# Kernel tuning notes

Measured on AMD Instinct MI355X. Metric: run time of the kernel, lower is better.

## Reference

```python
import jax, jax.numpy as jnp
import numpy as np

N_NODES = 50000
IN_C, HID_C, OUT_C = 128, 128, 64
N_EDGES = 800000


def setup_inputs() -> dict:
    key = jax.random.key(0)
    k1, k2, k3, k4, k5, k6 = jax.random.split(key, 6)
    x = jax.random.normal(k1, (N_NODES, IN_C), dtype=jnp.float32)
    edge_index = jax.random.randint(k2, (2, N_EDGES), 0, N_NODES, dtype=jnp.int64)
    # Glorot-ish init for the two GCN layer weights + biases
    W1 = jax.random.normal(k3, (IN_C, HID_C), dtype=jnp.float32) / np.sqrt(IN_C)
    b1 = jnp.zeros((HID_C,), dtype=jnp.float32)
    W2 = jax.random.normal(k4, (HID_C, OUT_C), dtype=jnp.float32) / np.sqrt(HID_C)
    b2 = jnp.zeros((OUT_C,), dtype=jnp.float32)
    return {"x": x, "edge_index": edge_index, "W1": W1, "b1": b1, "W2": W2, "b2": b2}


def _gcn_norm(edge_index, num_nodes):
    # Add self-loops, then symmetric normalization: deg^-1/2[row] * deg^-1/2[col]
    loops = jnp.arange(num_nodes, dtype=edge_index.dtype)
    row = jnp.concatenate([edge_index[0], loops])  # target nodes
    col = jnp.concatenate([edge_index[1], loops])  # source nodes
    ones = jnp.ones(row.shape[0], dtype=jnp.float32)
    deg = jax.ops.segment_sum(ones, row, num_segments=num_nodes)
    dinv = jnp.where(deg > 0, jax.lax.rsqrt(jnp.maximum(deg, 1.0)), 0.0)
    norm = dinv[row] * dinv[col]  # [E + N]
    return row, col, norm


def _gcn_conv(x, row, col, norm, W, b, num_nodes):
    h = x @ W                              # [N, C_out] — transform first (fewer FLOPs)
    msg = h[col] * norm[:, None]           # gather + scale  [E+N, C_out]
    out = jax.ops.segment_sum(msg, row, num_segments=num_nodes)  # scatter-add
    return out + b


def reference(x, edge_index, W1, b1, W2, b2):
    n = x.shape[0]
    row, col, norm = _gcn_norm(edge_index, n)
    h = _gcn_conv(x, row, col, norm, W1, b1, n)
    # original applies x.relu() then non_linearity (ReLU()) — idempotent, one relu suffices
    h = jax.nn.relu(h)
    return _gcn_conv(h, row, col, norm, W2, b2, n)
```

## Files before the change

### kernel.cpp

```cpp
#include <hip/hip_runtime.h>


#define CHUNKS 256
#define CAP    7168

typedef short bf16x8 __attribute__((ext_vector_type(8)));
typedef float f32x4 __attribute__((ext_vector_type(4)));

__device__ __forceinline__ float bf2f(unsigned int u16) {
    return __uint_as_float(u16 << 16);
}
__device__ __forceinline__ unsigned int f2bf_rne(float f) {
    unsigned int u = __float_as_uint(f);
    return (u + 0x7fffu + ((u >> 16) & 1u)) >> 16;
}
__device__ __forceinline__ unsigned int pack2bf(float a, float b) {
    return f2bf_rne(a) | (f2bf_rne(b) << 16);
}
__device__ __forceinline__ void add8(float* acc, uint4 p) {
    acc[0] += bf2f(p.x & 0xffffu); acc[1] += bf2f(p.x >> 16);
    acc[2] += bf2f(p.y & 0xffffu); acc[3] += bf2f(p.y >> 16);
    acc[4] += bf2f(p.z & 0xffffu); acc[5] += bf2f(p.z >> 16);
    acc[6] += bf2f(p.w & 0xffffu); acc[7] += bf2f(p.w >> 16);
}

__global__ __launch_bounds__(256) void p1_kernel(
    const int* __restrict__ row, const int* __restrict__ col, int E, int CE, int NB,
    const float* __restrict__ W1, const float* __restrict__ W2,
    unsigned short* __restrict__ Wt1, unsigned short* __restrict__ Wt2,
    int* __restrict__ pos, unsigned int* __restrict__ bucketc)
{
    __shared__ int hist[256], scn[256], cur[256];
    const int c = blockIdx.x, t = threadIdx.x;
    const int s = c * CE, e = min(E, s + CE);

    hist[t] = 0;
    __syncthreads();
    for (int i = s + t; i < e; i += 256) atomicAdd(&hist[row[i] >> 8], 1);
    {
        int i = c * 256 + t;
        if (i < 128 * 128) {
            int k = i >> 7, cc = i & 127;
            Wt1[cc * 128 + k] = (unsigned short)f2bf_rne(W1[i]);
        } else if (i < 128 * 128 + 128 * 64) {
            int j = i - 128 * 128;
            int k = j >> 6, cc = j & 63;
            Wt2[cc * 128 + k] = (unsigned short)f2bf_rne(W2[j]);
        }
    }
    __syncthreads();

    int v = hist[t];
    scn[t] = v;
    __syncthreads();
    #pragma unroll
    for (int d = 1; d < 256; d <<= 1) {
        int xv = (t >= d) ? scn[t - d] : 0;
        __syncthreads();
        scn[t] += xv;
        __syncthreads();
    }
    int excl = scn[t] - v;
    if (t <= NB) pos[t * CHUNKS + c] = excl;
    cur[t] = excl;
    __syncthreads();

    for (int i = s + t; i < e; i += 256) {
        int r = row[i];
        int p = atomicAdd(&cur[r >> 8], 1);
        bucketc[s + p] = (unsigned)(r & 255) | ((unsigned)col[i] << 8);
    }
}

__global__ __launch_bounds__(256) void p2_kernel(
    const int* __restrict__ pos, const unsigned int* __restrict__ bucketc,
    unsigned int* __restrict__ csrf, float* __restrict__ dinv,
    int4* __restrict__ nod, int N, int CE)
{
    __shared__ unsigned int ent[CAP];
    __shared__ int stmp[256], hist[256], scn[256], cnt2[256], smtot[1];
    const int b = blockIdx.x, t = threadIdx.x;

    const int p0 = pos[b * CHUNKS + t];
    const int p1 = pos[(b + 1) * CHUNKS + t];
    const int cnt = p1 - p0;

    stmp[t] = cnt;
    hist[t] = 0;
    cnt2[t] = 0;
    __syncthreads();
    #pragma unroll
    for (int d = 1; d < 256; d <<= 1) {
        int xv = (t >= d) ? stmp[t - d] : 0;
        __syncthreads();
        stmp[t] += xv;
        __syncthreads();
    }
    const int fbase = stmp[t] - cnt;
    if (t == 255) smtot[0] = stmp[255];
    __syncthreads();
    const int m = min(smtot[0], CAP);

    {
        const int src = t * CE + p0;
        int i = 0;
        for (; i + 1 < cnt; i += 2) {
            unsigned int u0 = bucketc[src + i];
            unsigned int u1 = bucketc[src + i + 1];
            int d0 = fbase + i;
            if (d0 + 1 < CAP) {
                ent[d0] = u0; ent[d0 + 1] = u1;
                atomicAdd(&hist[u0 & 255u], 1);
                atomicAdd(&hist[u1 & 255u], 1);
            }
        }
        if (i < cnt) {
            unsigned int u0 = bucketc[src + i];
            int d0 = fbase + i;
            if (d0 < CAP) {
                ent[d0] = u0;
                atomicAdd(&hist[u0 & 255u], 1);
            }
        }
    }
    __syncthreads();

    int h = hist[t];
    scn[t] = h;
    __syncthreads();
    #pragma unroll
    for (int d = 1; d < 256; d <<= 1) {
        int xv = (t >= d) ? scn[t - d] : 0;
        __syncthreads();
        scn[t] += xv;
        __syncthreads();
    }
    int base = scn[t] - h;

    int node = b * 256 + t;
    if (node < N) {
        float dv = rsqrtf((float)(h + 1));
        dinv[node] = dv;
        nod[node] = make_int4(b * CAP + base, b * CAP + base + h, __float_as_int(dv), 0);
    }
    scn[t] = base;
    __syncthreads();

    for (int i = t; i < m; i += 256) {
        unsigned int v = ent[i];
        int r = v & 255u;
        int slot = atomicAdd(&cnt2[r], 1);
        csrf[b * CAP + scn[r] + slot] = v >> 8;
    }
}


template <int CT, bool BF16IN>
__global__ __launch_bounds__(256) void gemm_mfma_kernel(
    const void* __restrict__ Xv, const unsigned short* __restrict__ Wt,
    const float* __restrict__ dinv, unsigned short* __restrict__ out, int N)
{
    constexpr int COUT = CT * 64;
    __shared__ unsigned short As[64 * 128];
    __shared__ unsigned short Bs[COUT * 128];
    __shared__ float dl[64];

    const int t = threadIdx.x;
    const int m0 = blockIdx.x * 64;

    if (BF16IN) {
        const unsigned short* X = (const unsigned short*)Xv;
        #pragma unroll
        for (int i = 0; i < 4; ++i) {
            int f = i * 256 + t;
            int r = f >> 4, c16 = f & 15;
            int rg = m0 + r;
            uint4 p = (rg < N) ? ((const uint4*)X)[(size_t)rg * 16 + c16]
                               : make_uint4(0u, 0u, 0u, 0u);
            int cb = c16 * 16;
            *(uint4*)((char*)As + r * 256 + (cb ^ ((r & 7) << 4))) = p;
        }
    } else {
        const float* X = (const float*)Xv;
        #pragma unroll
        for (int i = 0; i < 8; ++i) {
            int f = i * 256 + t;
            int r = f >> 5, c4 = f & 31;
            int rg = m0 + r;
            float4 v = (rg < N) ? ((const float4*)X)[(size_t)rg * 32 + c4]
                                : make_float4(0.f, 0.f, 0.f, 0.f);
            uint2 p;
            p.x = pack2bf(v.x, v.y);
            p.y = pack2bf(v.z, v.w);
            int cb = c4 * 8;
            *(uint2*)((char*)As + r * 256 + (cb ^ ((r & 7) << 4))) = p;
        }
    }
    #pragma unroll
    for (int i = 0; i < CT * 8; ++i) {
        int f = i * 256 + t;
        int r = f >> 5;
        int cb = (f & 31) * 8;
        uint2 p = ((const uint2*)Wt)[f];
        *(uint2*)((char*)Bs + r * 256 + (cb ^ ((r & 7) << 4))) = p;
    }
    if (t < 64) dl[t] = (m0 + t < N) ? dinv[m0 + t] : 0.f;
    __syncthreads();

    const int w = t >> 6, l = t & 63;
    const int lr = l & 15, lk = l >> 4;

    bf16x8 af[4][4];
    #pragma unroll
    for (int mt = 0; mt < 4; ++mt)
        #pragma unroll
        for (int kt = 0; kt < 4; ++kt) {
            int r = mt * 16 + lr;
            int cb = kt * 64 + lk * 16;
            af[mt][kt] = *(const bf16x8*)((const char*)As + r * 256 + (cb ^ ((r & 7) << 4)));
        }
    bf16x8 bfr[CT][4];
    #pragma unroll
    for (int ct = 0; ct < CT; ++ct)
        #pragma unroll
        for (int kt = 0; kt < 4; ++kt) {
            int c = w * (CT * 16) + ct * 16 + lr;
            int cb = kt * 64 + lk * 16;
            bfr[ct][kt] = *(const bf16x8*)((const char*)Bs + c * 256 + (cb ^ ((c & 7) << 4)));
        }

    f32x4 acc[4][CT];
    #pragma unroll
    for (int mt = 0; mt < 4; ++mt)
        #pragma unroll
        for (int ct = 0; ct < CT; ++ct)
            acc[mt][ct] = f32x4{0.f, 0.f, 0.f, 0.f};

    #pragma unroll
    for (int kt = 0; kt < 4; ++kt)
        #pragma unroll
        for (int mt = 0; mt < 4; ++mt)
            #pragma unroll
            for (int ct = 0; ct < CT; ++ct)
                acc[mt][ct] = __builtin_amdgcn_mfma_f32_16x16x32_bf16(
                    af[mt][kt], bfr[ct][kt], acc[mt][ct], 0, 0, 0);

    #pragma unroll
    for (int mt = 0; mt < 4; ++mt) {
        #pragma unroll
        for (int ct = 0; ct < CT; ++ct) {
            #pragma unroll
            for (int r = 0; r < 4; ++r) {
                int rowl = mt * 16 + lk * 4 + r;
                int grow = m0 + rowl;
                if (grow < N) {
                    int c = w * (CT * 16) + ct * 16 + lr;
                    float v = acc[mt][ct][r] * dl[rowl];
                    out[(size_t)grow * COUT + c] = (unsigned short)f2bf_rne(v);
                }
            }
        }
    }
}


__global__ __launch_bounds__(256) void agg1_kernel(
    const unsigned short* __restrict__ hs, const unsigned int* __restrict__ csr,
    const int4* __restrict__ nod, const float* __restrict__ bias,
    unsigned short* __restrict__ out, int N)
{
    const int w = threadIdx.x >> 6, l = threadIdx.x & 63;
    const int n = blockIdx.x * 4 + w;
    if (n >= N) return;
    const int q = l & 15, g = l >> 4;

    int4 se = nod[n];
    float acc[8] = {};
    if (g == 0)
        add8(acc, *(const uint4*)&hs[(size_t)n * 128 + q * 8]);

    int j = se.x + g;
    const int e = se.y;
    for (; j + 4 < e; j += 8) {
        int c0 = csr[j], c1 = csr[j + 4];
        uint4 p0 = *(const uint4*)&hs[(size_t)c0 * 128 + q * 8];
        uint4 p1 = *(const uint4*)&hs[(size_t)c1 * 128 + q * 8];
        add8(acc, p0);
        add8(acc, p1);
    }
    if (j < e)
        add8(acc, *(const uint4*)&hs[(size_t)csr[j] * 128 + q * 8]);

    #pragma unroll
    for (int i = 0; i < 8; ++i) {
        acc[i] += __shfl_xor(acc[i], 16);
        acc[i] += __shfl_xor(acc[i], 32);
    }

    if (g == 0) {
        float d = __int_as_float(se.z);
        float4 b0 = ((const float4*)bias)[q * 2];
        float4 b1 = ((const float4*)bias)[q * 2 + 1];
        float v0 = fmaxf(d * acc[0] + b0.x, 0.f), v1 = fmaxf(d * acc[1] + b0.y, 0.f);
        float v2 = fmaxf(d * acc[2] + b0.z, 0.f), v3 = fmaxf(d * acc[3] + b0.w, 0.f);
        float v4 = fmaxf(d * acc[4] + b1.x, 0.f), v5 = fmaxf(d * acc[5] + b1.y, 0.f);
        float v6 = fmaxf(d * acc[6] + b1.z, 0.f), v7 = fmaxf(d * acc[7] + b1.w, 0.f);
        uint4 o;
        o.x = pack2bf(v0, v1); o.y = pack2bf(v2, v3);
        o.z = pack2bf(v4, v5); o.w = pack2bf(v6, v7);
        *(uint4*)&out[(size_t)n * 128 + q * 8] = o;
    }
}

__global__ __launch_bounds__(256) void agg2_kernel(
    const unsigned short* __restrict__ hs, const unsigned int* __restrict__ csr,
    const int4* __restrict__ nod, const float* __restrict__ bias,
    float* __restrict__ out, int N)
{
    const int w = threadIdx.x >> 6, l = threadIdx.x & 63;
    const int n = blockIdx.x * 4 + w;
    if (n >= N) return;
    const int q = l & 7, g = l >> 3;

    int4 se = nod[n];
    float acc[8] = {};
    if (g == 0)
        add8(acc, *(const uint4*)&hs[(size_t)n * 64 + q * 8]);

    int j = se.x + g;
    const int e = se.y;
    for (; j + 8 < e; j += 16) {
        int c0 = csr[j], c1 = csr[j + 8];
        uint4 p0 = *(const uint4*)&hs[(size_t)c0 * 64 + q * 8];
        uint4 p1 = *(const uint4*)&hs[(size_t)c1 * 64 + q * 8];
        add8(acc, p0);
        add8(acc, p1);
    }
    if (j < e)
        add8(acc, *(const uint4*)&hs[(size_t)csr[j] * 64 + q * 8]);

    #pragma unroll
    for (int i = 0; i < 8; ++i) {
        acc[i] += __shfl_xor(acc[i], 8);
        acc[i] += __shfl_xor(acc[i], 16);
        acc[i] += __shfl_xor(acc[i], 32);
    }

    if (g == 0) {
        float d = __int_as_float(se.z);
        float4 b0 = ((const float4*)bias)[q * 2];
        float4 b1 = ((const float4*)bias)[q * 2 + 1];
        float4 o0, o1;
        o0.x = d * acc[0] + b0.x; o0.y = d * acc[1] + b0.y;
        o0.z = d * acc[2] + b0.z; o0.w = d * acc[3] + b0.w;
        o1.x = d * acc[4] + b1.x; o1.y = d * acc[5] + b1.y;
        o1.z = d * acc[6] + b1.z; o1.w = d * acc[7] + b1.w;
        *(float4*)&out[(size_t)n * 64 + q * 8] = o0;
        *(float4*)&out[(size_t)n * 64 + q * 8 + 4] = o1;
    }
}

extern "C" void kernel_launch(void* const* d_in, const int* in_sizes, int n_in,
                              void* d_out, int out_size, void* d_ws, size_t ws_size,
                              hipStream_t stream)
{
    const float* x  = (const float*)d_in[0];
    const int*   ei = (const int*)d_in[1];
    const float* W1 = (const float*)d_in[2];
    const float* b1 = (const float*)d_in[3];
    const float* W2 = (const float*)d_in[4];
    const float* b2 = (const float*)d_in[5];
    float* out = (float*)d_out;

    const int N = in_sizes[0] / 128;
    const int E = in_sizes[1] / 2;
    const int* row = ei;
    const int* col = ei + E;
    const int NB = (N + 255) / 256;
    const int CE = (E + CHUNKS - 1) / CHUNKS;

    char* ws = (char*)d_ws;
    size_t o = 0;
    auto take = [&](size_t bytes) { void* p = ws + o; o = (o + bytes + 255) & ~(size_t)255; return p; };
    int*   pos    = (int*)  take((size_t)(NB + 1) * CHUNKS * 4);
    unsigned int* bucketc = (unsigned int*)take((size_t)E * 4);
    unsigned int* csrf    = (unsigned int*)take((size_t)NB * CAP * 4);
    float* dinv   = (float*)take((size_t)N * 4);
    int4*  nod    = (int4*) take((size_t)N * 16);
    unsigned short* Wt1 = (unsigned short*)take(128 * 128 * 2);
    unsigned short* Wt2 = (unsigned short*)take(64 * 128 * 2);
    unsigned short* hs  = (unsigned short*)take((size_t)N * 128 * 2);
    unsigned short* a1  = (unsigned short*)take((size_t)N * 128 * 2);
    unsigned short* hs2 = hs;

    p1_kernel<<<CHUNKS, 256, 0, stream>>>(row, col, E, CE, NB, W1, W2, Wt1, Wt2,
                                          pos, bucketc);
    p2_kernel<<<NB, 256, 0, stream>>>(pos, bucketc, csrf, dinv, nod, N, CE);

    gemm_mfma_kernel<2, false><<<(N + 63) / 64, 256, 0, stream>>>(x, Wt1, dinv, hs, N);
    agg1_kernel<<<(N + 3) / 4, 256, 0, stream>>>(hs, csrf, nod, b1, a1, N);

    gemm_mfma_kernel<1, true><<<(N + 63) / 64, 256, 0, stream>>>(a1, Wt2, dinv, hs2, N);
    agg2_kernel<<<(N + 3) / 4, 256, 0, stream>>>(hs2, csrf, nod, b2, out, N);
}
```

Measured before the change: 109.1 us.

## Fuse layer-1 aggregation with layer-2 GEMM in one kernel

The first-layer aggregation (gather, bias, ReLU) now writes its bf16 output tile into shared memory, and the same 1024-thread block immediately runs the 64x128 by 128x64 MFMA for layer 2 and writes the dinv-scaled hs2. This removes the a1 intermediate round-trip through global memory and one kernel launch. The aggregation mapping also changes from four edge groups per wave with a shuffle reduction to one 16-lane group per node. That drops the shuffles but gives each node less memory-level parallelism, and the larger blocks may lower occupancy on the latency-bound gather.

```diff
diff --git a/kernel.cpp b/kernel.cpp
--- a/kernel.cpp
+++ b/kernel.cpp
@@ -154,13 +154,11 @@
     }
 }
 
-
-template <int CT, bool BF16IN>
 __global__ __launch_bounds__(256) void gemm_mfma_kernel(
-    const void* __restrict__ Xv, const unsigned short* __restrict__ Wt,
+    const float* __restrict__ X, const unsigned short* __restrict__ Wt,
     const float* __restrict__ dinv, unsigned short* __restrict__ out, int N)
 {
-    constexpr int COUT = CT * 64;
+    constexpr int COUT = 128;
     __shared__ unsigned short As[64 * 128];
     __shared__ unsigned short Bs[COUT * 128];
     __shared__ float dl[64];
@@ -168,36 +166,21 @@
     const int t = threadIdx.x;
     const int m0 = blockIdx.x * 64;
 
-    if (BF16IN) {
-        const unsigned short* X = (const unsigned short*)Xv;
-        #pragma unroll
-        for (int i = 0; i < 4; ++i) {
-            int f = i * 256 + t;
-            int r = f >> 4, c16 = f & 15;
-            int rg = m0 + r;
-            uint4 p = (rg < N) ? ((const uint4*)X)[(size_t)rg * 16 + c16]
-                               : make_uint4(0u, 0u, 0u, 0u);
-            int cb = c16 * 16;
-            *(uint4*)((char*)As + r * 256 + (cb ^ ((r & 7) << 4))) = p;
-        }
-    } else {
-        const float* X = (const float*)Xv;
-        #pragma unroll
-        for (int i = 0; i < 8; ++i) {
-            int f = i * 256 + t;
-            int r = f >> 5, c4 = f & 31;
-            int rg = m0 + r;
-            float4 v = (rg < N) ? ((const float4*)X)[(size_t)rg * 32 + c4]
-                                : make_float4(0.f, 0.f, 0.f, 0.f);
-            uint2 p;
-            p.x = pack2bf(v.x, v.y);
-            p.y = pack2bf(v.z, v.w);
-            int cb = c4 * 8;
-            *(uint2*)((char*)As + r * 256 + (cb ^ ((r & 7) << 4))) = p;
-        }
-    }
-    #pragma unroll
-    for (int i = 0; i < CT * 8; ++i) {
+    #pragma unroll
+    for (int i = 0; i < 8; ++i) {
+        int f = i * 256 + t;
+        int r = f >> 5, c4 = f & 31;
+        int rg = m0 + r;
+        float4 v = (rg < N) ? ((const float4*)X)[(size_t)rg * 32 + c4]
+                            : make_float4(0.f, 0.f, 0.f, 0.f);
+        uint2 p;
+        p.x = pack2bf(v.x, v.y);
+        p.y = pack2bf(v.z, v.w);
+        int cb = c4 * 8;
+        *(uint2*)((char*)As + r * 256 + (cb ^ ((r & 7) << 4))) = p;
+    }
+    #pragma unroll
+    for (int i = 0; i < 16; ++i) {
         int f = i * 256 + t;
         int r = f >> 5;
         int cb = (f & 31) * 8;
@@ -219,21 +202,21 @@
             int cb = kt * 64 + lk * 16;
             af[mt][kt] = *(const bf16x8*)((const char*)As + r * 256 + (cb ^ ((r & 7) << 4)));
         }
-    bf16x8 bfr[CT][4];
-    #pragma unroll
-    for (int ct = 0; ct < CT; ++ct)
+    bf16x8 bfr[2][4];
+    #pragma unroll
+    for (int ct = 0; ct < 2; ++ct)
         #pragma unroll
         for (int kt = 0; kt < 4; ++kt) {
-            int c = w * (CT * 16) + ct * 16 + lr;
+            int c = w * 32 + ct * 16 + lr;
             int cb = kt * 64 + lk * 16;
             bfr[ct][kt] = *(const bf16x8*)((const char*)Bs + c * 256 + (cb ^ ((c & 7) << 4)));
         }
 
-    f32x4 acc[4][CT];
+    f32x4 acc[4][2];
     #pragma unroll
     for (int mt = 0; mt < 4; ++mt)
         #pragma unroll
-        for (int ct = 0; ct < CT; ++ct)
+        for (int ct = 0; ct < 2; ++ct)
             acc[mt][ct] = f32x4{0.f, 0.f, 0.f, 0.f};
 
     #pragma unroll
@@ -241,20 +224,20 @@
         #pragma unroll
         for (int mt = 0; mt < 4; ++mt)
             #pragma unroll
-            for (int ct = 0; ct < CT; ++ct)
+            for (int ct = 0; ct < 2; ++ct)
                 acc[mt][ct] = __builtin_amdgcn_mfma_f32_16x16x32_bf16(
                     af[mt][kt], bfr[ct][kt], acc[mt][ct], 0, 0, 0);
 
     #pragma unroll
     for (int mt = 0; mt < 4; ++mt) {
         #pragma unroll
-        for (int ct = 0; ct < CT; ++ct) {
+        for (int ct = 0; ct < 2; ++ct) {
             #pragma unroll
             for (int r = 0; r < 4; ++r) {
                 int rowl = mt * 16 + lk * 4 + r;
                 int grow = m0 + rowl;
                 if (grow < N) {
-                    int c = w * (CT * 16) + ct * 16 + lr;
+                    int c = w * 32 + ct * 16 + lr;
                     float v = acc[mt][ct][r] * dl[rowl];
                     out[(size_t)grow * COUT + c] = (unsigned short)f2bf_rne(v);
                 }
@@ -263,52 +246,90 @@
     }
 }
 
-
-__global__ __launch_bounds__(256) void agg1_kernel(
+__global__ __launch_bounds__(1024) void agg1g2_kernel(
     const unsigned short* __restrict__ hs, const unsigned int* __restrict__ csr,
-    const int4* __restrict__ nod, const float* __restrict__ bias,
-    unsigned short* __restrict__ out, int N)
-{
-    const int w = threadIdx.x >> 6, l = threadIdx.x & 63;
-    const int n = blockIdx.x * 4 + w;
-    if (n >= N) return;
-    const int q = l & 15, g = l >> 4;
-
-    int4 se = nod[n];
+    const int4* __restrict__ nod, const float* __restrict__ bias ,
+    const unsigned short* __restrict__ Wt2, unsigned short* __restrict__ hs2, int N)
+{
+    __shared__ unsigned short As[64 * 128];
+    __shared__ unsigned short Bs[64 * 128];
+    __shared__ float dl[64];
+
+    const int t = threadIdx.x;
+    const int w = t >> 6, l = t & 63;
+    const int n0 = blockIdx.x * 64;
+    const int sub = l >> 4, q = l & 15;
+    const int rowl = w * 4 + sub;
+    const int n = n0 + rowl;
+
+    {
+        int r = t >> 4;
+        int cb = (t & 15) * 16;
+        uint4 p = ((const uint4*)Wt2)[t];
+        *(uint4*)((char*)Bs + r * 256 + (cb ^ ((r & 7) << 4))) = p;
+    }
+
     float acc[8] = {};
-    if (g == 0)
+    float dv = 0.f;
+    if (n < N) {
+        int4 se = nod[n];
+        dv = __int_as_float(se.z);
         add8(acc, *(const uint4*)&hs[(size_t)n * 128 + q * 8]);
-
-    int j = se.x + g;
-    const int e = se.y;
-    for (; j + 4 < e; j += 8) {
-        int c0 = csr[j], c1 = csr[j + 4];
-        uint4 p0 = *(const uint4*)&hs[(size_t)c0 * 128 + q * 8];
-        uint4 p1 = *(const uint4*)&hs[(size_t)c1 * 128 + q * 8];
-        add8(acc, p0);
-        add8(acc, p1);
-    }
-    if (j < e)
-        add8(acc, *(const uint4*)&hs[(size_t)csr[j] * 128 + q * 8]);
-
-    #pragma unroll
-    for (int i = 0; i < 8; ++i) {
-        acc[i] += __shfl_xor(acc[i], 16);
-        acc[i] += __shfl_xor(acc[i], 32);
-    }
-
-    if (g == 0) {
-        float d = __int_as_float(se.z);
+        int j = se.x;
+        const int e = se.y;
+        for (; j + 1 < e; j += 2) {
+            int c0 = csr[j], c1 = csr[j + 1];
+            uint4 p0 = *(const uint4*)&hs[(size_t)c0 * 128 + q * 8];
+            uint4 p1 = *(const uint4*)&hs[(size_t)c1 * 128 + q * 8];
+            add8(acc, p0);
+            add8(acc, p1);
+        }
+        if (j < e)
+            add8(acc, *(const uint4*)&hs[(size_t)csr[j] * 128 + q * 8]);
+    }
+
+    {
         float4 b0 = ((const float4*)bias)[q * 2];
-        float4 b1 = ((const float4*)bias)[q * 2 + 1];
-        float v0 = fmaxf(d * acc[0] + b0.x, 0.f), v1 = fmaxf(d * acc[1] + b0.y, 0.f);
-        float v2 = fmaxf(d * acc[2] + b0.z, 0.f), v3 = fmaxf(d * acc[3] + b0.w, 0.f);
-        float v4 = fmaxf(d * acc[4] + b1.x, 0.f), v5 = fmaxf(d * acc[5] + b1.y, 0.f);
-        float v6 = fmaxf(d * acc[6] + b1.z, 0.f), v7 = fmaxf(d * acc[7] + b1.w, 0.f);
+        float4 b1v = ((const float4*)bias)[q * 2 + 1];
+        float v0 = fmaxf(dv * acc[0] + b0.x, 0.f), v1 = fmaxf(dv * acc[1] + b0.y, 0.f);
+        float v2 = fmaxf(dv * acc[2] + b0.z, 0.f), v3 = fmaxf(dv * acc[3] + b0.w, 0.f);
+        float v4 = fmaxf(dv * acc[4] + b1v.x, 0.f), v5 = fmaxf(dv * acc[5] + b1v.y, 0.f);
+        float v6 = fmaxf(dv * acc[6] + b1v.z, 0.f), v7 = fmaxf(dv * acc[7] + b1v.w, 0.f);
         uint4 o;
         o.x = pack2bf(v0, v1); o.y = pack2bf(v2, v3);
         o.z = pack2bf(v4, v5); o.w = pack2bf(v6, v7);
-        *(uint4*)&out[(size_t)n * 128 + q * 8] = o;
+        int cb = q * 16;
+        *(uint4*)((char*)As + rowl * 256 + (cb ^ ((rowl & 7) << 4))) = o;
+        if (q == 0) dl[rowl] = dv;
+    }
+    __syncthreads();
+
+    const int lr = l & 15, lk = l >> 4;
+    const int mt = w >> 2, ct = w & 3;
+
+    bf16x8 af[4], bfr[4];
+    #pragma unroll
+    for (int kt = 0; kt < 4; ++kt) {
+        int r = mt * 16 + lr;
+        int cb = kt * 64 + lk * 16;
+        af[kt] = *(const bf16x8*)((const char*)As + r * 256 + (cb ^ ((r & 7) << 4)));
+        int c = ct * 16 + lr;
+        bfr[kt] = *(const bf16x8*)((const char*)Bs + c * 256 + (cb ^ ((c & 7) << 4)));
+    }
+    f32x4 a = f32x4{0.f, 0.f, 0.f, 0.f};
+    #pragma unroll
+    for (int kt = 0; kt < 4; ++kt)
+        a = __builtin_amdgcn_mfma_f32_16x16x32_bf16(af[kt], bfr[kt], a, 0, 0, 0);
+
+    #pragma unroll
+    for (int r = 0; r < 4; ++r) {
+        int rowm = mt * 16 + lk * 4 + r;
+        int grow = n0 + rowm;
+        if (grow < N) {
+            int c = ct * 16 + lr;
+            float v = a[r] * dl[rowm];
+            hs2[(size_t)grow * 64 + c] = (unsigned short)f2bf_rne(v);
+        }
     }
 }
 
@@ -390,16 +411,15 @@
     unsigned short* Wt1 = (unsigned short*)take(128 * 128 * 2);
     unsigned short* Wt2 = (unsigned short*)take(64 * 128 * 2);
     unsigned short* hs  = (unsigned short*)take((size_t)N * 128 * 2);
-    unsigned short* a1  = (unsigned short*)take((size_t)N * 128 * 2);
-    unsigned short* hs2 = hs;
+    unsigned short* hs2 = (unsigned short*)take((size_t)N * 64 * 2);
 
     p1_kernel<<<CHUNKS, 256, 0, stream>>>(row, col, E, CE, NB, W1, W2, Wt1, Wt2,
                                           pos, bucketc);
     p2_kernel<<<NB, 256, 0, stream>>>(pos, bucketc, csrf, dinv, nod, N, CE);
 
-    gemm_mfma_kernel<2, false><<<(N + 63) / 64, 256, 0, stream>>>(x, Wt1, dinv, hs, N);
-    agg1_kernel<<<(N + 3) / 4, 256, 0, stream>>>(hs, csrf, nod, b1, a1, N);
-
-    gemm_mfma_kernel<1, true><<<(N + 63) / 64, 256, 0, stream>>>(a1, Wt2, dinv, hs2, N);
+    gemm_mfma_kernel<<<(N + 63) / 64, 256, 0, stream>>>(x, Wt1, dinv, hs, N);
+
+    agg1g2_kernel<<<(N + 63) / 64, 1024, 0, stream>>>(hs, csrf, nod, b1, Wt2, hs2, N);
+
     agg2_kernel<<<(N + 3) / 4, 256, 0, stream>>>(hs2, csrf, nod, b2, out, N);
 }
```

Result: faster. 103.0 us (-5.6%).
